# Optimization experiments

Measured on AMD Instinct MI355X. Metric: run time of the kernel, lower is better.

Reference implementation:

```python
import jax, jax.numpy as jnp
import numpy as np

NUM_HEADS = 8
EMBED_DIM = 512


def _attention(q, k, v, mask=None):
    # q,k,v: [batch, heads, Lq, d] / [batch, heads, Lk, d]
    s = jnp.einsum('bhqd,bhkd->bhqk', q, k)
    if mask is not None:
        s = jnp.where(mask, jnp.asarray(-1000.0, s.dtype), s)
    p = jax.nn.softmax(s, axis=-1)
    return jnp.einsum('bhqk,bhkd->bhqd', p, v)


def _t_mask(T, H):
    # True where attention is DISALLOWED (query frame t_q < key frame t_k)
    tq = jnp.arange(T)[:, None]
    tk = jnp.arange(T)[None, :]
    blocked = tq < tk  # [T, T]
    m = jnp.repeat(jnp.repeat(blocked, H, axis=0), H, axis=1)  # [T*H, T*H]
    return m


def setup_inputs() -> dict:
    key = jax.random.key(0)
    ks = jax.random.split(key, 10)
    B, T, H, W, E = 4, 4, 28, 28, EMBED_DIM
    N = T * H * W
    s_in = (2.0 / (E + 3 * E)) ** 0.5  # xavier-ish
    s_sq = (1.0 / E) ** 0.5
    return {
        'x': jax.random.normal(ks[0], (B, N, E), dtype=jnp.float32),
        'in_proj_weight': jax.random.normal(ks[1], (3 * E, E), dtype=jnp.float32) * s_in,
        'in_proj_bias': jnp.zeros((3 * E,), dtype=jnp.float32),
        'out_proj_w': jax.random.normal(ks[2], (E, E), dtype=jnp.float32) * s_sq,
        'out_proj_b': jnp.zeros((E,), dtype=jnp.float32),
        'in_proj_weight_t': jax.random.normal(ks[3], (E, E), dtype=jnp.float32) * s_sq,
        'in_proj_bias_t': jnp.zeros((E,), dtype=jnp.float32),
        'out_proj_t_w': jax.random.normal(ks[4], (E, E), dtype=jnp.float32) * s_sq,
        'out_proj_t_b': jnp.zeros((E,), dtype=jnp.float32),
        'alpha': 0.0001 * jnp.ones((E,), dtype=jnp.float32),
        'H': 28,
        'W': 28,
    }


def reference(x, in_proj_weight, in_proj_bias, out_proj_w, out_proj_b,
              in_proj_weight_t, in_proj_bias_t, out_proj_t_w, out_proj_t_b,
              alpha, H, W):
    B, N, C = x.shape
    nh = NUM_HEADS
    hc = C // nh
    T = N // (H * W)
    scale = hc ** (-0.5)

    # ---- spatial (per-frame) attention: _forward_2d ----
    qkv = x @ in_proj_weight.T + in_proj_bias            # [B, N, 3C]
    qkv = qkv.reshape(B, T, H * W, 3, nh, hc)
    qkv = qkv.transpose(3, 0, 1, 4, 2, 5).reshape(3, B * T, nh, H * W, hc)
    q, k, v = qkv[0], qkv[1], qkv[2]
    o = _attention(q * scale, k, v)                       # [B*T, nh, HW, hc]
    xs = o.transpose(0, 2, 1, 3).reshape(B, N, C)
    xs = xs @ out_proj_w.T + out_proj_b

    ks = jax.lax.stop_gradient(k)                         # detached cache
    vs = jax.lax.stop_gradient(v)

    # ---- axial temporal attention ----
    q_t = (x @ in_proj_weight_t.T + in_proj_bias_t) * scale  # [B, N, C]
    q_t = q_t.reshape(B, T, H, W, nh, hc)
    q_th = q_t.transpose(0, 3, 4, 1, 2, 5).reshape(B * W, nh, T * H, hc)
    q_tw = q_t.transpose(0, 2, 4, 1, 3, 5).reshape(B * H, nh, T * W, hc)

    k6 = ks.reshape(B, T, nh, H, W, hc)
    v6 = vs.reshape(B, T, nh, H, W, hc)
    k_th = k6.transpose(0, 4, 2, 1, 3, 5).reshape(B * W, nh, T * H, hc)
    k_tw = k6.transpose(0, 3, 2, 1, 4, 5).reshape(B * H, nh, T * W, hc)
    v_th = v6.transpose(0, 4, 2, 1, 3, 5).reshape(B * W, nh, T * H, hc)
    v_tw = v6.transpose(0, 3, 2, 1, 4, 5).reshape(B * H, nh, T * W, hc)

    o_th = _attention(q_th, k_th, v_th, _t_mask(T, H))    # [B*W, nh, T*H, hc]
    o_tw = _attention(q_tw, k_tw, v_tw, _t_mask(T, W))    # [B*H, nh, T*W, hc]

    o_th = o_th.reshape(B, W, nh, T, H, hc).transpose(0, 3, 4, 1, 2, 5).reshape(B, N, C)
    o_tw = o_tw.reshape(B, H, nh, T, W, hc).transpose(0, 3, 1, 4, 2, 5).reshape(B, N, C)

    x_t = (o_th + o_tw) @ out_proj_t_w.T + out_proj_t_b
    return xs + alpha * x_t
```

## Files before the change

kernel.cpp:

```cpp
#include <hip/hip_runtime.h>
#include <stdint.h>

#define NN   3136
#define MM   12544
#define SCALE 0.125f
#define KSCL  (0.125f * 1.44269504088896f)
#define MASKED (-30000.0f)

typedef __attribute__((ext_vector_type(8))) unsigned short ushort8;
typedef __attribute__((ext_vector_type(8))) short short8;
typedef __attribute__((ext_vector_type(4))) float floatx4;

__device__ __forceinline__ float b2f(unsigned short u) {
    union { unsigned int i; float f; } x; x.i = ((unsigned int)u) << 16; return x.f;
}
__device__ __forceinline__ unsigned short f2b(float f) {
    union { float f; unsigned int i; } x; x.f = f;
    unsigned int r = x.i + 0x7fffu + ((x.i >> 16) & 1u);
    return (unsigned short)(r >> 16);
}
__device__ __forceinline__ float fexp2(float x) {
    return __builtin_amdgcn_exp2f(x);
}
__device__ __forceinline__ void load8(const void* p, size_t e, int isf32, float o[8]) {
    if (isf32) {
        const float* f = (const float*)p + e;
        #pragma unroll
        for (int i = 0; i < 8; ++i) o[i] = f[i];
    } else {
        ushort8 u = *(const ushort8*)((const unsigned short*)p + e);
        #pragma unroll
        for (int i = 0; i < 8; ++i) o[i] = b2f(u[i]);
    }
}
__device__ __forceinline__ float load1(const void* p, int e, int isf32) {
    return isf32 ? ((const float*)p)[e] : b2f(((const unsigned short*)p)[e]);
}

__global__ void detect_dtype(const void* __restrict__ x, int* __restrict__ flagp)
{
    if (threadIdx.x == 0 && blockIdx.x == 0) {
        const unsigned short* u = (const unsigned short*)x;
        int c = 0;
        for (int i = 0; i < 512; ++i) {
            const float v = b2f(u[i]);
            if (!(v == v) || fabsf(v) > 1000.0f) ++c;
        }
        *flagp = (c >= 16) ? 1 : 0;
    }
}

__global__ __launch_bounds__(256) void convert_x(
    const int* __restrict__ flagp, const float* __restrict__ x,
    unsigned short* __restrict__ xb)
{
    if (!*flagp) return;
    const size_t i = ((size_t)blockIdx.x * 256 + threadIdx.x) * 8;
    const float4 a = *(const float4*)(x + i);
    const float4 b = *(const float4*)(x + i + 4);
    ushort8 o;
    o[0] = f2b(a.x); o[1] = f2b(a.y); o[2] = f2b(a.z); o[3] = f2b(a.w);
    o[4] = f2b(b.x); o[5] = f2b(b.y); o[6] = f2b(b.z); o[7] = f2b(b.w);
    *(ushort8*)(xb + i) = o;
}

__global__ __launch_bounds__(256) void convert_wp(
    const int* __restrict__ flagp, const void* __restrict__ Wi,
    const void* __restrict__ Wt, unsigned short* __restrict__ wp)
{
    const int isf32 = *flagp;
    const size_t e = ((size_t)blockIdx.x * 256 + threadIdx.x) * 8;
    const int row = (int)(e >> 9);
    const int col = (int)(e & 511);
    float v[8];
    if (row < 1536) load8(Wi, (size_t)row * 512 + col, isf32, v);
    else            load8(Wt, (size_t)(row - 1536) * 512 + col, isf32, v);
    if (row >= 512 && row < 1024) {
        #pragma unroll
        for (int u = 0; u < 8; ++u) v[u] *= KSCL;
    }
    ushort8 o;
    #pragma unroll
    for (int u = 0; u < 8; ++u) o[u] = f2b(v[u]);
    *(ushort8*)(wp + e) = o;
}

__global__ __launch_bounds__(256) void convert_wf(
    const int* __restrict__ flagp, const void* __restrict__ Wo,
    const void* __restrict__ Wto, const void* __restrict__ alp,
    unsigned short* __restrict__ qkv)
{
    const int isf32 = *flagp;
    const size_t e = ((size_t)blockIdx.x * 256 + threadIdx.x) * 8;
    const int row = (int)(e >> 10);
    const int k = (int)(e & 1023);
    float v[8];
    if (k < 512) load8(Wo, (size_t)row * 512 + k, isf32, v);
    else {
        const float a = load1(alp, row, isf32);
        load8(Wto, (size_t)row * 512 + (k - 512), isf32, v);
        #pragma unroll
        for (int u = 0; u < 8; ++u) v[u] *= a;
    }
    ushort8 o;
    #pragma unroll
    for (int u = 0; u < 8; ++u) o[u] = f2b(v[u]);
    *(ushort8*)(qkv + (size_t)row * 1536 + 512 + k) = o;
}

__global__ __launch_bounds__(256) void gemm_proj_mfma(
    const int* __restrict__ flagp, const void* __restrict__ x,
    const unsigned short* __restrict__ xb,
    const unsigned short* __restrict__ wp,
    const void* __restrict__ bi, const void* __restrict__ bt,
    unsigned short* __restrict__ qkv, unsigned short* __restrict__ qt)
{
    __shared__ unsigned short A_sh[128][40];
    __shared__ unsigned short B_sh[64][40];
    const int gid = blockIdx.x;
    const int mt = (gid >> 8) * 8 + (gid & 7);
    const int nt = (gid & 255) >> 3;
    if (mt >= 98) return;
    const int m0 = mt * 128, n0 = nt * 64;

    const int isf32 = *flagp;
    const unsigned short* A = isf32 ? xb : (const unsigned short*)x;
    const int tid = threadIdx.x, lane = tid & 63, wv = tid >> 6;
    const int lane15 = lane & 15, quad = lane >> 4;
    const int wm = wv >> 1, wn = wv & 1;

    const int ra = tid >> 1, ca = (tid & 1) * 16;
    const int rb = tid >> 2, cb = (tid & 3) * 8;
    const int nb = n0 + rb;

    floatx4 acc[4][2];
    #pragma unroll
    for (int i = 0; i < 4; ++i)
        #pragma unroll
        for (int j = 0; j < 2; ++j) acc[i][j] = (floatx4){0.f,0.f,0.f,0.f};

    for (int k0 = 0; k0 < 512; k0 += 32) {
        const unsigned short* ap = A + (size_t)(m0 + ra) * 512 + k0 + ca;
        *(ushort8*)&A_sh[ra][ca]     = *(const ushort8*)ap;
        *(ushort8*)&A_sh[ra][ca + 8] = *(const ushort8*)(ap + 8);
        *(ushort8*)&B_sh[rb][cb] = *(const ushort8*)(wp + (size_t)nb * 512 + k0 + cb);
        __syncthreads();

        short8 af[4], bf[2];
        #pragma unroll
        for (int i = 0; i < 4; ++i)
            af[i] = *(const short8*)&A_sh[wm * 64 + i * 16 + lane15][quad * 8];
        #pragma unroll
        for (int j = 0; j < 2; ++j)
            bf[j] = *(const short8*)&B_sh[wn * 32 + j * 16 + lane15][quad * 8];
        #pragma unroll
        for (int i = 0; i < 4; ++i)
            #pragma unroll
            for (int j = 0; j < 2; ++j)
                acc[i][j] = __builtin_amdgcn_mfma_f32_16x16x32_bf16(af[i], bf[j], acc[i][j], 0, 0, 0);
        __syncthreads();
    }

    #pragma unroll
    for (int j = 0; j < 2; ++j) {
        const int col = n0 + wn * 32 + j * 16 + lane15;
        float bias;
        unsigned short* dst;
        int stride;
        if (col < 1536) {
            bias = load1(bi, col, isf32);
            if (col >= 512 && col < 1024) bias *= KSCL;
            dst = qkv; stride = 1536;
        }
        else { bias = load1(bt, col - 1536, isf32); dst = qt; stride = 512; }
        const int cofs = (col < 1536) ? col : (col - 1536);
        #pragma unroll
        for (int i = 0; i < 4; ++i)
            #pragma unroll
            for (int r = 0; r < 4; ++r) {
                const int m = m0 + wm * 64 + i * 16 + quad * 4 + r;
                dst[(size_t)m * stride + cofs] = f2b(acc[i][j][r] + bias);
            }
    }
}

__global__ __launch_bounds__(256) void gemm_final_mfma(
    const int* __restrict__ flagp,
    const unsigned short* __restrict__ qkv, const unsigned short* __restrict__ qt,
    const void* __restrict__ bo, const void* __restrict__ bto,
    const void* __restrict__ alp, void* __restrict__ outp)
{
    __shared__ unsigned short A_sh[128][40];
    __shared__ unsigned short B_sh[64][40];
    const int gid = blockIdx.x;
    const int mt = (gid >> 6) * 8 + (gid & 7);
    const int nt = (gid & 63) >> 3;
    if (mt >= 98) return;
    const int m0 = mt * 128, n0 = nt * 64;

    const int isf32 = *flagp;
    const int tid = threadIdx.x, lane = tid & 63, wv = tid >> 6;
    const int lane15 = lane & 15, quad = lane >> 4;
    const int wm = wv >> 1, wn = wv & 1;

    const int ra = tid >> 1, ca = (tid & 1) * 16;
    const int rb = tid >> 2, cb = (tid & 3) * 8;
    const int nb = n0 + rb;

    floatx4 acc[4][2];
    #pragma unroll
    for (int i = 0; i < 4; ++i)
        #pragma unroll
        for (int j = 0; j < 2; ++j) acc[i][j] = (floatx4){0.f,0.f,0.f,0.f};

    for (int k0 = 0; k0 < 1024; k0 += 32) {
        const int m = m0 + ra;
        const unsigned short* ap = (k0 < 512)
            ? qkv + (size_t)m * 1536 + k0 + ca
            : qt  + (size_t)m * 512  + (k0 - 512) + ca;
        *(ushort8*)&A_sh[ra][ca]     = *(const ushort8*)ap;
        *(ushort8*)&A_sh[ra][ca + 8] = *(const ushort8*)(ap + 8);
        *(ushort8*)&B_sh[rb][cb] =
            *(const ushort8*)(qkv + (size_t)nb * 1536 + 512 + k0 + cb);
        __syncthreads();

        short8 af[4], bf[2];
        #pragma unroll
        for (int i = 0; i < 4; ++i)
            af[i] = *(const short8*)&A_sh[wm * 64 + i * 16 + lane15][quad * 8];
        #pragma unroll
        for (int j = 0; j < 2; ++j)
            bf[j] = *(const short8*)&B_sh[wn * 32 + j * 16 + lane15][quad * 8];
        #pragma unroll
        for (int i = 0; i < 4; ++i)
            #pragma unroll
            for (int j = 0; j < 2; ++j)
                acc[i][j] = __builtin_amdgcn_mfma_f32_16x16x32_bf16(af[i], bf[j], acc[i][j], 0, 0, 0);
        __syncthreads();
    }

    #pragma unroll
    for (int j = 0; j < 2; ++j) {
        const int col = n0 + wn * 32 + j * 16 + lane15;
        const float bias = load1(bo, col, isf32) + load1(alp, col, isf32) * load1(bto, col, isf32);
        #pragma unroll
        for (int i = 0; i < 4; ++i)
            #pragma unroll
            for (int r = 0; r < 4; ++r) {
                const int m = m0 + wm * 64 + i * 16 + quad * 4 + r;
                const float val = acc[i][j][r] + bias;
                const size_t idx = (size_t)m * 512 + col;
                if (isf32) ((float*)outp)[idx] = val;
                else       ((unsigned short*)outp)[idx] = f2b(val);
            }
    }
}

__global__ __launch_bounds__(512) void attn_spatial_mfma(unsigned short* __restrict__ qkv)
{
    __shared__ unsigned short K_sh[64][72];
    __shared__ unsigned short VT_sh[64][72];
    __shared__ unsigned short P_sh[8][16][72];

    const int tid = threadIdx.x, lane = tid & 63, wv = tid >> 6;
    const int lane15 = lane & 15, quad = lane >> 4;

    const int gid = blockIdx.x;
    const int xcd = gid & 7, kk = gid >> 3;
    const int grp = xcd * 16 + kk / 7;
    const int qb  = kk % 7;
    const int head = grp & 7, bt = grp >> 3;

    const int t0 = qb * 8 + wv;
    const bool act = (t0 < 49);
    const int q0 = act ? t0 * 16 : 0;
    const int frame0 = bt * 784;

    short8 q_lo = {0,0,0,0,0,0,0,0}, q_hi = {0,0,0,0,0,0,0,0};
    if (act) {
        const unsigned short* qp = qkv + (size_t)(frame0 + q0 + lane15) * 1536 + head * 64 + quad * 8;
        q_lo = *(const short8*)qp;
        q_hi = *(const short8*)(qp + 32);
    }

    floatx4 accO[4] = {{0.f,0.f,0.f,0.f},{0.f,0.f,0.f,0.f},{0.f,0.f,0.f,0.f},{0.f,0.f,0.f,0.f}};
    float ls[4] = {0.f, 0.f, 0.f, 0.f};

    const int key_l = tid & 63;
    const int cs    = (tid >> 6) * 8;
    const int swzp  = (lane15 >> 2) << 4;

    for (int kt = 0; kt < 13; ++kt) {
        __syncthreads();
        const int key = kt * 64 + key_l;
        ushort8 k8 = {0,0,0,0,0,0,0,0}, v8 = {0,0,0,0,0,0,0,0};
        if (key < 784) {
            const unsigned short* kp = qkv + (size_t)(frame0 + key) * 1536 + head * 64 + cs;
            k8 = *(const ushort8*)(kp + 512);
            v8 = *(const ushort8*)(kp + 1024);
        }
        *(ushort8*)&K_sh[key_l][cs] = k8;
        #pragma unroll
        for (int u = 0; u < 8; ++u) VT_sh[cs + u][key_l] = v8[u];
        __syncthreads();

        floatx4 s[4];
        #pragma unroll
        for (int st = 0; st < 4; ++st) {
            const short8 kfl = *(const short8*)&K_sh[st * 16 + lane15][quad * 8];
            const short8 kfh = *(const short8*)&K_sh[st * 16 + lane15][32 + quad * 8];
            floatx4 a = {0.f,0.f,0.f,0.f};
            a = __builtin_amdgcn_mfma_f32_16x16x32_bf16(q_lo, kfl, a, 0, 0, 0);
            a = __builtin_amdgcn_mfma_f32_16x16x32_bf16(q_hi, kfh, a, 0, 0, 0);
            s[st] = a;
        }

        const bool tail = (kt == 12);
        #pragma unroll
        for (int st = 0; st < 4; ++st)
            #pragma unroll
            for (int r = 0; r < 4; ++r) {
                const float v = (tail && st >= 1) ? MASKED : s[st][r];
                const float p = fexp2(v);
                ls[r] += p;
                P_sh[wv][quad * 4 + r][(st * 16 + lane15) ^ (quad << 4)] = f2b(p);
            }

        #pragma unroll
        for (int kc = 0; kc < 2; ++kc) {
            const short8 pf = *(const short8*)&P_sh[wv][lane15][(kc * 32 + quad * 8) ^ swzp];
            #pragma unroll
            for (int nt = 0; nt < 4; ++nt) {
                const short8 vf = *(const short8*)&VT_sh[nt * 16 + lane15][kc * 32 + quad * 8];
                accO[nt] = __builtin_amdgcn_mfma_f32_16x16x32_bf16(pf, vf, accO[nt], 0, 0, 0);
            }
        }
    }

    #pragma unroll
    for (int off = 1; off < 16; off <<= 1)
        #pragma unroll
        for (int r = 0; r < 4; ++r)
            ls[r] += __shfl_xor(ls[r], off, 64);

    if (act) {
        #pragma unroll
        for (int nt = 0; nt < 4; ++nt)
            #pragma unroll
            for (int r = 0; r < 4; ++r) {
                const int qrow = q0 + quad * 4 + r;
                qkv[(size_t)(frame0 + qrow) * 1536 + head * 64 + nt * 16 + lane15]
                    = f2b(accO[nt][r] / ls[r]);
            }
    }
}

__global__ __launch_bounds__(448) void attn_axial(
    const unsigned short* __restrict__ qkv, const unsigned short* __restrict__ qtu,
    const unsigned short* __restrict__ oth, unsigned short* __restrict__ outp,
    const int pass)
{
    __shared__ unsigned short K_sh[112][72];
    __shared__ unsigned short VT_sh[64][136];
    __shared__ unsigned short P_sh[7][16][136];

    const int tid = threadIdx.x, lane = tid & 63, wv = tid >> 6;
    const int lane15 = lane & 15, quad = lane >> 4;
    const int b = blockIdx.x / 28, pos = blockIdx.x % 28;
    const int head = blockIdx.y;
    const int swzp = (lane15 >> 2) << 4;

    for (int idx = tid; idx < 1024; idx += 448) {
        const int j = idx >> 3, cc = (idx & 7) << 3;
        if (j < 112) {
            const int tk = j / 28, rk = j % 28;
            const int n_k = tk * 784 + (pass == 0 ? rk * 28 + pos : pos * 28 + rk);
            const unsigned short* kp = qkv + (size_t)(b * NN + n_k) * 1536 + 512 + head * 64 + cc;
            const ushort8 k8 = *(const ushort8*)kp;
            const ushort8 v8 = *(const ushort8*)(kp + 512);
            *(ushort8*)&K_sh[j][cc] = k8;
            #pragma unroll
            for (int u = 0; u < 8; ++u) VT_sh[cc + u][j ^ cc] = v8[u];
        } else {
            #pragma unroll
            for (int u = 0; u < 8; ++u) VT_sh[cc + u][j ^ cc] = 0;
        }
    }
    __syncthreads();

    const int tile = wv;
    {
        const int iq = tile * 16 + lane15;
        const int tq_q = iq / 28, rq = iq % 28;
        const int n_q = tq_q * 784 + (pass == 0 ? rq * 28 + pos : pos * 28 + rq);
        const size_t qaddr = (size_t)(b * NN + n_q) * 512 + head * 64;
        const short8 q_lo = *(const short8*)(qtu + qaddr + quad * 8);
        const short8 q_hi = *(const short8*)(qtu + qaddr + 32 + quad * 8);

        floatx4 s[7];
        #pragma unroll
        for (int st = 0; st < 7; ++st) {
            const short8 kfl = *(const short8*)&K_sh[st * 16 + lane15][quad * 8];
            const short8 kfh = *(const short8*)&K_sh[st * 16 + lane15][32 + quad * 8];
            floatx4 acc = {0.f,0.f,0.f,0.f};
            acc = __builtin_amdgcn_mfma_f32_16x16x32_bf16(q_lo, kfl, acc, 0, 0, 0);
            acc = __builtin_amdgcn_mfma_f32_16x16x32_bf16(q_hi, kfh, acc, 0, 0, 0);
            s[st] = acc;
        }

        int tq_row[4];
        #pragma unroll
        for (int r = 0; r < 4; ++r) tq_row[r] = (tile * 16 + quad * 4 + r) / 28;
        float l[4] = {0.f, 0.f, 0.f, 0.f};
        #pragma unroll
        for (int st = 0; st < 7; ++st) {
            const int tk = (st * 16 + lane15) / 28;
            #pragma unroll
            for (int r = 0; r < 4; ++r) {
                const float v = (tk <= tq_row[r]) ? s[st][r] : MASKED;
                const float p = fexp2(v);
                s[st][r] = p;
                l[r] += p;
            }
        }
        #pragma unroll
        for (int off = 1; off < 16; off <<= 1)
            #pragma unroll
            for (int r = 0; r < 4; ++r)
                l[r] += __shfl_xor(l[r], off, 64);

        #pragma unroll
        for (int r = 0; r < 4; ++r) {
            const int row = quad * 4 + r;
            #pragma unroll
            for (int st = 0; st < 7; ++st)
                P_sh[wv][row][(st * 16 + lane15) ^ (quad << 4)] = f2b(s[st][r]);
            P_sh[wv][row][(112 + lane15) ^ (quad << 4)] = 0;
        }

        floatx4 accO[4] = {{0.f,0.f,0.f,0.f},{0.f,0.f,0.f,0.f},{0.f,0.f,0.f,0.f},{0.f,0.f,0.f,0.f}};
        #pragma unroll
        for (int kc = 0; kc < 4; ++kc) {
            const short8 pf = *(const short8*)&P_sh[wv][lane15][(kc * 32 + quad * 8) ^ swzp];
            #pragma unroll
            for (int nt = 0; nt < 4; ++nt) {
                const int row = nt * 16 + lane15;
                const short8 vf = *(const short8*)&VT_sh[row][(kc * 32 + quad * 8) ^ ((row >> 3) << 3)];
                accO[nt] = __builtin_amdgcn_mfma_f32_16x16x32_bf16(pf, vf, accO[nt], 0, 0, 0);
            }
        }

        #pragma unroll
        for (int r = 0; r < 4; ++r) {
            const int io = tile * 16 + quad * 4 + r;
            const int to = io / 28, ro = io % 28;
            const int n_o = to * 784 + (pass == 0 ? ro * 28 + pos : pos * 28 + ro);
            const size_t oaddr = (size_t)(b * NN + n_o) * 512 + head * 64;
            #pragma unroll
            for (int nt = 0; nt < 4; ++nt) {
                float o = accO[nt][r] / l[r];
                if (pass == 1) o += b2f(oth[oaddr + nt * 16 + lane15]);
                outp[oaddr + nt * 16 + lane15] = f2b(o);
            }
        }
    }
}

__global__ void fill_val(unsigned short* o, unsigned short v, int n) {
    const int i = blockIdx.x * 256 + threadIdx.x;
    if (i < n) o[i] = v;
}

extern "C" void kernel_launch(void* const* d_in, const int* in_sizes, int n_in,
                              void* d_out, int out_size, void* d_ws, size_t ws_size,
                              hipStream_t stream)
{
    const void* x   = d_in[0];
    const void* Wi  = d_in[1];
    const void* bi  = d_in[2];
    const void* Wo  = d_in[3];
    const void* bo  = d_in[4];
    const void* Wt  = d_in[5];
    const void* bt  = d_in[6];
    const void* Wto = d_in[7];
    const void* bto = d_in[8];
    const void* alp = d_in[9];

    const size_t QKV_ELEMS = (size_t)MM * 1536;
    const size_t QT_ELEMS  = (size_t)MM * 512;
    const size_t FLAG_OFF  = (QKV_ELEMS + QT_ELEMS) * 2;
    const size_t NEED      = FLAG_OFF + 256;

    if (ws_size < NEED) {
        fill_val<<<dim3((out_size + 255) / 256), dim3(256), 0, stream>>>(
            (unsigned short*)d_out, (unsigned short)0x3f80, out_size);
        return;
    }

    unsigned short* qkv = (unsigned short*)d_ws;
    unsigned short* qt  = qkv + QKV_ELEMS;
    int* flagp = (int*)((char*)d_ws + FLAG_OFF);
    unsigned short* oth = (unsigned short*)d_out;
    unsigned short* xb  = oth + (size_t)MM * 512;
    unsigned short* wp  = oth;

    dim3 blk(256);
    detect_dtype<<<dim3(1), dim3(64), 0, stream>>>(x, flagp);
    convert_x<<<dim3(MM * 512 / (256 * 8)), blk, 0, stream>>>(flagp, (const float*)x, xb);
    convert_wp<<<dim3(2048 * 512 / (256 * 8)), blk, 0, stream>>>(flagp, Wi, Wt, wp);
    gemm_proj_mfma<<<dim3(13 * 256), blk, 0, stream>>>(
        flagp, x, xb, wp, bi, bt, qkv, qt);
    attn_spatial_mfma<<<dim3(112 * 8), dim3(512), 0, stream>>>(qkv);
    attn_axial<<<dim3(112, 8), dim3(448), 0, stream>>>(qkv, qt, nullptr, oth, 0);
    attn_axial<<<dim3(112, 8), dim3(448), 0, stream>>>(qkv, qt, oth, qt, 1);
    convert_wf<<<dim3(512 * 1024 / (256 * 8)), blk, 0, stream>>>(flagp, Wo, Wto, alp, qkv);
    gemm_final_mfma<<<dim3(13 * 64), blk, 0, stream>>>(
        flagp, qkv, qt, bo, bto, alp, d_out);
}
```

Before: 297.4 us.

## Stage spatial-attention K/V in two large LDS halves with XOR swizzling

The spatial attention kernel now loads 448 keys and then the remaining 336 keys (padded to 384) of K and transposed V into large shared-memory buffers. This replaces thirteen 64-key tiles that each needed two barriers, so the kernel hits far fewer __syncthreads. K and VT stores and reads are XOR-swizzled to avoid LDS bank conflicts without padding. The cost is much larger LDS use per block (roughly 64KB+ for K_sh plus VT_sh), which limits occupancy to one block per CU. Load and compute are also no longer overlapped across tiles.

Result: slower. 308.9 us (+3.9%).

```diff
diff --git a/kernel.cpp b/kernel.cpp
--- a/kernel.cpp
+++ b/kernel.cpp
@@ -258,8 +258,8 @@
 
 __global__ __launch_bounds__(512) void attn_spatial_mfma(unsigned short* __restrict__ qkv)
 {
-    __shared__ unsigned short K_sh[64][72];
-    __shared__ unsigned short VT_sh[64][72];
+    __shared__ unsigned short K_sh[448][72];
+    __shared__ unsigned short VT_sh[64][448];
     __shared__ unsigned short P_sh[8][16][72];
 
     const int tid = threadIdx.x, lane = tid & 63, wv = tid >> 6;
@@ -286,55 +286,73 @@
     floatx4 accO[4] = {{0.f,0.f,0.f,0.f},{0.f,0.f,0.f,0.f},{0.f,0.f,0.f,0.f},{0.f,0.f,0.f,0.f}};
     float ls[4] = {0.f, 0.f, 0.f, 0.f};
 
-    const int key_l = tid & 63;
-    const int cs    = (tid >> 6) * 8;
-    const int swzp  = (lane15 >> 2) << 4;
-
-    for (int kt = 0; kt < 13; ++kt) {
-        __syncthreads();
-        const int key = kt * 64 + key_l;
-        ushort8 k8 = {0,0,0,0,0,0,0,0}, v8 = {0,0,0,0,0,0,0,0};
-        if (key < 784) {
-            const unsigned short* kp = qkv + (size_t)(frame0 + key) * 1536 + head * 64 + cs;
-            k8 = *(const ushort8*)(kp + 512);
-            v8 = *(const ushort8*)(kp + 1024);
-        }
-        *(ushort8*)&K_sh[key_l][cs] = k8;
-        #pragma unroll
-        for (int u = 0; u < 8; ++u) VT_sh[cs + u][key_l] = v8[u];
-        __syncthreads();
-
+    const int swzp = (lane15 >> 2) << 4;
+    const int r7l  = lane15 & 7;
+
+    auto chunk = [&](int c, bool msk) {
         floatx4 s[4];
         #pragma unroll
         for (int st = 0; st < 4; ++st) {
-            const short8 kfl = *(const short8*)&K_sh[st * 16 + lane15][quad * 8];
-            const short8 kfh = *(const short8*)&K_sh[st * 16 + lane15][32 + quad * 8];
+            const int row = c * 64 + st * 16 + lane15;
+            const short8 kfl = *(const short8*)&K_sh[row][(quad ^ r7l) * 8];
+            const short8 kfh = *(const short8*)&K_sh[row][((quad + 4) ^ r7l) * 8];
             floatx4 a = {0.f,0.f,0.f,0.f};
             a = __builtin_amdgcn_mfma_f32_16x16x32_bf16(q_lo, kfl, a, 0, 0, 0);
             a = __builtin_amdgcn_mfma_f32_16x16x32_bf16(q_hi, kfh, a, 0, 0, 0);
             s[st] = a;
         }
-
-        const bool tail = (kt == 12);
         #pragma unroll
         for (int st = 0; st < 4; ++st)
             #pragma unroll
             for (int r = 0; r < 4; ++r) {
-                const float v = (tail && st >= 1) ? MASKED : s[st][r];
+                const float v = (msk && st >= 1) ? MASKED : s[st][r];
                 const float p = fexp2(v);
                 ls[r] += p;
                 P_sh[wv][quad * 4 + r][(st * 16 + lane15) ^ (quad << 4)] = f2b(p);
             }
-
         #pragma unroll
         for (int kc = 0; kc < 2; ++kc) {
             const short8 pf = *(const short8*)&P_sh[wv][lane15][(kc * 32 + quad * 8) ^ swzp];
             #pragma unroll
             for (int nt = 0; nt < 4; ++nt) {
-                const short8 vf = *(const short8*)&VT_sh[nt * 16 + lane15][kc * 32 + quad * 8];
+                const int vrow = nt * 16 + lane15;
+                const short8 vf = *(const short8*)
+                    &VT_sh[vrow][(c * 64 + kc * 32 + quad * 8) ^ ((vrow >> 3) << 3)];
                 accO[nt] = __builtin_amdgcn_mfma_f32_16x16x32_bf16(pf, vf, accO[nt], 0, 0, 0);
             }
         }
+    };
+
+    for (int idx = tid; idx < 448 * 8; idx += 512) {
+        const int j = idx >> 3, cc = idx & 7, d0 = cc * 8;
+        const unsigned short* kp = qkv + (size_t)(frame0 + j) * 1536 + head * 64 + d0;
+        const ushort8 k8 = *(const ushort8*)(kp + 512);
+        const ushort8 v8 = *(const ushort8*)(kp + 1024);
+        *(ushort8*)&K_sh[j][(cc ^ (j & 7)) * 8] = k8;
+        #pragma unroll
+        for (int u = 0; u < 8; ++u) VT_sh[d0 + u][j ^ (cc << 3)] = v8[u];
+    }
+    __syncthreads();
+    if (act) {
+        for (int c = 0; c < 7; ++c) chunk(c, false);
+    }
+    __syncthreads();
+
+    for (int idx = tid; idx < 384 * 8; idx += 512) {
+        const int j = idx >> 3, cc = idx & 7, d0 = cc * 8;
+        ushort8 k8 = {0,0,0,0,0,0,0,0}, v8 = {0,0,0,0,0,0,0,0};
+        if (j < 336) {
+            const unsigned short* kp = qkv + (size_t)(frame0 + 448 + j) * 1536 + head * 64 + d0;
+            k8 = *(const ushort8*)(kp + 512);
+            v8 = *(const ushort8*)(kp + 1024);
+        }
+        *(ushort8*)&K_sh[j][(cc ^ (j & 7)) * 8] = k8;
+        #pragma unroll
+        for (int u = 0; u < 8; ++u) VT_sh[d0 + u][j ^ (cc << 3)] = v8[u];
+    }
+    __syncthreads();
+    if (act) {
+        for (int c = 0; c < 6; ++c) chunk(c, c == 5);
     }
 
     #pragma unroll
```

## Fuse spatial attention with first axial pass and merge pre-conversion kernels

Applied to the files above, without the earlier changes.

Spatial attention and the first axial attention pass become one launch. Interleaved slabs of blocks run either the spatial or the axial body out of a shared 64000-byte static LDS buffer. The two are independent: spatial writes only the Q slots, and axial reads only K/V and qt. The x conversion and the weight conversion kernels are also merged into one launch. The intent is to cut launch overhead and tail idle time and to let the two attention workloads overlap. The cost is a larger fixed LDS footprint per block, which may lower the occupancy of the spatial blocks.

Measured after the change: 319.2 us. 7.3% more time.

```diff
diff --git a/kernel.cpp b/kernel.cpp
--- a/kernel.cpp
+++ b/kernel.cpp
@@ -50,39 +50,39 @@
     }
 }
 
-__global__ __launch_bounds__(256) void convert_x(
+__global__ __launch_bounds__(256) void pre_convert(
     const int* __restrict__ flagp, const float* __restrict__ x,
-    unsigned short* __restrict__ xb)
-{
-    if (!*flagp) return;
-    const size_t i = ((size_t)blockIdx.x * 256 + threadIdx.x) * 8;
-    const float4 a = *(const float4*)(x + i);
-    const float4 b = *(const float4*)(x + i + 4);
-    ushort8 o;
-    o[0] = f2b(a.x); o[1] = f2b(a.y); o[2] = f2b(a.z); o[3] = f2b(a.w);
-    o[4] = f2b(b.x); o[5] = f2b(b.y); o[6] = f2b(b.z); o[7] = f2b(b.w);
-    *(ushort8*)(xb + i) = o;
-}
-
-__global__ __launch_bounds__(256) void convert_wp(
-    const int* __restrict__ flagp, const void* __restrict__ Wi,
-    const void* __restrict__ Wt, unsigned short* __restrict__ wp)
-{
+    unsigned short* __restrict__ xb,
+    const void* __restrict__ Wi, const void* __restrict__ Wt,
+    unsigned short* __restrict__ wp)
+{
+    const int g = blockIdx.x;
     const int isf32 = *flagp;
-    const size_t e = ((size_t)blockIdx.x * 256 + threadIdx.x) * 8;
-    const int row = (int)(e >> 9);
-    const int col = (int)(e & 511);
-    float v[8];
-    if (row < 1536) load8(Wi, (size_t)row * 512 + col, isf32, v);
-    else            load8(Wt, (size_t)(row - 1536) * 512 + col, isf32, v);
-    if (row >= 512 && row < 1024) {
-        #pragma unroll
-        for (int u = 0; u < 8; ++u) v[u] *= KSCL;
-    }
-    ushort8 o;
-    #pragma unroll
-    for (int u = 0; u < 8; ++u) o[u] = f2b(v[u]);
-    *(ushort8*)(wp + e) = o;
+    if (g < 3136) {
+        if (!isf32) return;
+        const size_t i = ((size_t)g * 256 + threadIdx.x) * 8;
+        const float4 a = *(const float4*)(x + i);
+        const float4 b = *(const float4*)(x + i + 4);
+        ushort8 o;
+        o[0] = f2b(a.x); o[1] = f2b(a.y); o[2] = f2b(a.z); o[3] = f2b(a.w);
+        o[4] = f2b(b.x); o[5] = f2b(b.y); o[6] = f2b(b.z); o[7] = f2b(b.w);
+        *(ushort8*)(xb + i) = o;
+    } else {
+        const size_t e = ((size_t)(g - 3136) * 256 + threadIdx.x) * 8;
+        const int row = (int)(e >> 9);
+        const int col = (int)(e & 511);
+        float v[8];
+        if (row < 1536) load8(Wi, (size_t)row * 512 + col, isf32, v);
+        else            load8(Wt, (size_t)(row - 1536) * 512 + col, isf32, v);
+        if (row >= 512 && row < 1024) {
+            #pragma unroll
+            for (int u = 0; u < 8; ++u) v[u] *= KSCL;
+        }
+        ushort8 o;
+        #pragma unroll
+        for (int u = 0; u < 8; ++u) o[u] = f2b(v[u]);
+        *(ushort8*)(wp + e) = o;
+    }
 }
 
 __global__ __launch_bounds__(256) void convert_wf(
@@ -256,17 +256,17 @@
     }
 }
 
-__global__ __launch_bounds__(512) void attn_spatial_mfma(unsigned short* __restrict__ qkv)
-{
-    __shared__ unsigned short K_sh[64][72];
-    __shared__ unsigned short VT_sh[64][72];
-    __shared__ unsigned short P_sh[8][16][72];
+__device__ __forceinline__ void spatial_body(
+    unsigned short* __restrict__ qkv, const int sub, unsigned char* smem)
+{
+    unsigned short (*K_sh)[72]      = (unsigned short (*)[72])smem;
+    unsigned short (*VT_sh)[72]     = (unsigned short (*)[72])(smem + 9216);
+    unsigned short (*P_sh)[16][72]  = (unsigned short (*)[16][72])(smem + 18432);
 
     const int tid = threadIdx.x, lane = tid & 63, wv = tid >> 6;
     const int lane15 = lane & 15, quad = lane >> 4;
 
-    const int gid = blockIdx.x;
-    const int xcd = gid & 7, kk = gid >> 3;
+    const int xcd = sub & 7, kk = sub >> 3;
     const int grp = xcd * 16 + kk / 7;
     const int qb  = kk % 7;
     const int head = grp & 7, bt = grp >> 3;
@@ -355,26 +355,25 @@
     }
 }
 
-__global__ __launch_bounds__(448) void attn_axial(
+__device__ __forceinline__ void axial0_body(
     const unsigned short* __restrict__ qkv, const unsigned short* __restrict__ qtu,
-    const unsigned short* __restrict__ oth, unsigned short* __restrict__ outp,
-    const int pass)
-{
-    __shared__ unsigned short K_sh[112][72];
-    __shared__ unsigned short VT_sh[64][136];
-    __shared__ unsigned short P_sh[7][16][136];
+    unsigned short* __restrict__ outp, const int sub, unsigned char* smem)
+{
+    unsigned short (*K_sh)[72]       = (unsigned short (*)[72])smem;
+    unsigned short (*VT_sh)[136]     = (unsigned short (*)[136])(smem + 16128);
+    unsigned short (*P_sh)[16][136]  = (unsigned short (*)[16][136])(smem + 33536);
 
     const int tid = threadIdx.x, lane = tid & 63, wv = tid >> 6;
     const int lane15 = lane & 15, quad = lane >> 4;
-    const int b = blockIdx.x / 28, pos = blockIdx.x % 28;
-    const int head = blockIdx.y;
+    const int head = sub / 112, xy = sub % 112;
+    const int b = xy / 28, pos = xy % 28;
     const int swzp = (lane15 >> 2) << 4;
 
-    for (int idx = tid; idx < 1024; idx += 448) {
+    for (int idx = tid; idx < 1024; idx += 512) {
         const int j = idx >> 3, cc = (idx & 7) << 3;
         if (j < 112) {
             const int tk = j / 28, rk = j % 28;
-            const int n_k = tk * 784 + (pass == 0 ? rk * 28 + pos : pos * 28 + rk);
+            const int n_k = tk * 784 + rk * 28 + pos;
             const unsigned short* kp = qkv + (size_t)(b * NN + n_k) * 1536 + 512 + head * 64 + cc;
             const ushort8 k8 = *(const ushort8*)kp;
             const ushort8 v8 = *(const ushort8*)(kp + 512);
@@ -388,11 +387,12 @@
     }
     __syncthreads();
 
+    if (wv >= 7) return;
     const int tile = wv;
     {
         const int iq = tile * 16 + lane15;
         const int tq_q = iq / 28, rq = iq % 28;
-        const int n_q = tq_q * 784 + (pass == 0 ? rq * 28 + pos : pos * 28 + rq);
+        const int n_q = tq_q * 784 + rq * 28 + pos;
         const size_t qaddr = (size_t)(b * NN + n_q) * 512 + head * 64;
         const short8 q_lo = *(const short8*)(qtu + qaddr + quad * 8);
         const short8 q_hi = *(const short8*)(qtu + qaddr + 32 + quad * 8);
@@ -454,12 +454,131 @@
         for (int r = 0; r < 4; ++r) {
             const int io = tile * 16 + quad * 4 + r;
             const int to = io / 28, ro = io % 28;
-            const int n_o = to * 784 + (pass == 0 ? ro * 28 + pos : pos * 28 + ro);
+            const int n_o = to * 784 + ro * 28 + pos;
+            const size_t oaddr = (size_t)(b * NN + n_o) * 512 + head * 64;
+            #pragma unroll
+            for (int nt = 0; nt < 4; ++nt)
+                outp[oaddr + nt * 16 + lane15] = f2b(accO[nt][r] / l[r]);
+        }
+    }
+}
+
+__global__ __launch_bounds__(512) void attn_fused(
+    unsigned short* __restrict__ qkv, const unsigned short* __restrict__ qtu,
+    unsigned short* __restrict__ oth)
+{
+    __shared__ __align__(16) unsigned char smem[64000];
+    const int g = blockIdx.x;
+    const int slab = g >> 3, lane8 = g & 7;
+    const int sub = (slab >> 1) * 8 + lane8;
+    if ((slab & 1) == 0) spatial_body(qkv, sub, smem);
+    else                 axial0_body(qkv, qtu, oth, sub, smem);
+}
+
+__global__ __launch_bounds__(448) void attn_axial1(
+    const unsigned short* __restrict__ qkv, const unsigned short* __restrict__ qtu,
+    const unsigned short* __restrict__ oth, unsigned short* __restrict__ outp)
+{
+    __shared__ unsigned short K_sh[112][72];
+    __shared__ unsigned short VT_sh[64][136];
+    __shared__ unsigned short P_sh[7][16][136];
+
+    const int tid = threadIdx.x, lane = tid & 63, wv = tid >> 6;
+    const int lane15 = lane & 15, quad = lane >> 4;
+    const int b = blockIdx.x / 28, pos = blockIdx.x % 28;
+    const int head = blockIdx.y;
+    const int swzp = (lane15 >> 2) << 4;
+
+    for (int idx = tid; idx < 1024; idx += 448) {
+        const int j = idx >> 3, cc = (idx & 7) << 3;
+        if (j < 112) {
+            const int tk = j / 28, rk = j % 28;
+            const int n_k = tk * 784 + pos * 28 + rk;
+            const unsigned short* kp = qkv + (size_t)(b * NN + n_k) * 1536 + 512 + head * 64 + cc;
+            const ushort8 k8 = *(const ushort8*)kp;
+            const ushort8 v8 = *(const ushort8*)(kp + 512);
+            *(ushort8*)&K_sh[j][cc] = k8;
+            #pragma unroll
+            for (int u = 0; u < 8; ++u) VT_sh[cc + u][j ^ cc] = v8[u];
+        } else {
+            #pragma unroll
+            for (int u = 0; u < 8; ++u) VT_sh[cc + u][j ^ cc] = 0;
+        }
+    }
+    __syncthreads();
+
+    const int tile = wv;
+    {
+        const int iq = tile * 16 + lane15;
+        const int tq_q = iq / 28, rq = iq % 28;
+        const int n_q = tq_q * 784 + pos * 28 + rq;
+        const size_t qaddr = (size_t)(b * NN + n_q) * 512 + head * 64;
+        const short8 q_lo = *(const short8*)(qtu + qaddr + quad * 8);
+        const short8 q_hi = *(const short8*)(qtu + qaddr + 32 + quad * 8);
+
+        floatx4 s[7];
+        #pragma unroll
+        for (int st = 0; st < 7; ++st) {
+            const short8 kfl = *(const short8*)&K_sh[st * 16 + lane15][quad * 8];
+            const short8 kfh = *(const short8*)&K_sh[st * 16 + lane15][32 + quad * 8];
+            floatx4 acc = {0.f,0.f,0.f,0.f};
+            acc = __builtin_amdgcn_mfma_f32_16x16x32_bf16(q_lo, kfl, acc, 0, 0, 0);
+            acc = __builtin_amdgcn_mfma_f32_16x16x32_bf16(q_hi, kfh, acc, 0, 0, 0);
+            s[st] = acc;
+        }
+
+        int tq_row[4];
+        #pragma unroll
+        for (int r = 0; r < 4; ++r) tq_row[r] = (tile * 16 + quad * 4 + r) / 28;
+        float l[4] = {0.f, 0.f, 0.f, 0.f};
+        #pragma unroll
+        for (int st = 0; st < 7; ++st) {
+            const int tk = (st * 16 + lane15) / 28;
+            #pragma unroll
+            for (int r = 0; r < 4; ++r) {
+                const float v = (tk <= tq_row[r]) ? s[st][r] : MASKED;
+                const float p = fexp2(v);
+                s[st][r] = p;
+                l[r] += p;
+            }
+        }
+        #pragma unroll
+        for (int off = 1; off < 16; off <<= 1)
+            #pragma unroll
+            for (int r = 0; r < 4; ++r)
+                l[r] += __shfl_xor(l[r], off, 64);
+
+        #pragma unroll
+        for (int r = 0; r < 4; ++r) {
+            const int row = quad * 4 + r;
+            #pragma unroll
+            for (int st = 0; st < 7; ++st)
+                P_sh[wv][row][(st * 16 + lane15) ^ (quad << 4)] = f2b(s[st][r]);
+            P_sh[wv][row][(112 + lane15) ^ (quad << 4)] = 0;
+        }
+
+        floatx4 accO[4] = {{0.f,0.f,0.f,0.f},{0.f,0.f,0.f,0.f},{0.f,0.f,0.f,0.f},{0.f,0.f,0.f,0.f}};
+        #pragma unroll
+        for (int kc = 0; kc < 4; ++kc) {
+            const short8 pf = *(const short8*)&P_sh[wv][lane15][(kc * 32 + quad * 8) ^ swzp];
+            #pragma unroll
+            for (int nt = 0; nt < 4; ++nt) {
+                const int row = nt * 16 + lane15;
+                const short8 vf = *(const short8*)&VT_sh[row][(kc * 32 + quad * 8) ^ ((row >> 3) << 3)];
+                accO[nt] = __builtin_amdgcn_mfma_f32_16x16x32_bf16(pf, vf, accO[nt], 0, 0, 0);
+            }
+        }
+
+        #pragma unroll
+        for (int r = 0; r < 4; ++r) {
+            const int io = tile * 16 + quad * 4 + r;
+            const int to = io / 28, ro = io % 28;
+            const int n_o = to * 784 + pos * 28 + ro;
             const size_t oaddr = (size_t)(b * NN + n_o) * 512 + head * 64;
             #pragma unroll
             for (int nt = 0; nt < 4; ++nt) {
                 float o = accO[nt][r] / l[r];
-                if (pass == 1) o += b2f(oth[oaddr + nt * 16 + lane15]);
+                o += b2f(oth[oaddr + nt * 16 + lane15]);
                 outp[oaddr + nt * 16 + lane15] = f2b(o);
             }
         }
@@ -506,13 +625,12 @@
 
     dim3 blk(256);
     detect_dtype<<<dim3(1), dim3(64), 0, stream>>>(x, flagp);
-    convert_x<<<dim3(MM * 512 / (256 * 8)), blk, 0, stream>>>(flagp, (const float*)x, xb);
-    convert_wp<<<dim3(2048 * 512 / (256 * 8)), blk, 0, stream>>>(flagp, Wi, Wt, wp);
+    pre_convert<<<dim3(3136 + 512), blk, 0, stream>>>(
+        flagp, (const float*)x, xb, Wi, Wt, wp);
     gemm_proj_mfma<<<dim3(13 * 256), blk, 0, stream>>>(
         flagp, x, xb, wp, bi, bt, qkv, qt);
-    attn_spatial_mfma<<<dim3(112 * 8), dim3(512), 0, stream>>>(qkv);
-    attn_axial<<<dim3(112, 8), dim3(448), 0, stream>>>(qkv, qt, nullptr, oth, 0);
-    attn_axial<<<dim3(112, 8), dim3(448), 0, stream>>>(qkv, qt, oth, qt, 1);
+    attn_fused<<<dim3(1792), dim3(512), 0, stream>>>(qkv, qt, oth);
+    attn_axial1<<<dim3(112, 8), dim3(448), 0, stream>>>(qkv, qt, oth, qt);
     convert_wf<<<dim3(512 * 1024 / (256 * 8)), blk, 0, stream>>>(flagp, Wo, Wto, alp, qkv);
     gemm_final_mfma<<<dim3(13 * 64), blk, 0, stream>>>(
         flagp, qkv, qt, bo, bto, alp, d_out);
```

## Double-buffer K/V tiles in spatial attention and merge conversion kernels

Applied to the files above, without the earlier changes.

The spatial attention kernel now keeps two shared-memory buffers for K and V^T. It prefetches the next key tile into registers while computing on the current one, which removes one barrier per iteration and hides global-load latency behind the MFMA work. Separately, the x and weight conversion kernels are merged into a single launch to save one kernel launch. The cost is doubled LDS for the K/V buffers, which could reduce occupancy, plus higher register pressure from the prefetched values.

Result: faster. 283.9 us (-4.6%).

```diff
diff --git a/kernel.cpp b/kernel.cpp
--- a/kernel.cpp
+++ b/kernel.cpp
@@ -50,39 +50,39 @@
     }
 }
 
-__global__ __launch_bounds__(256) void convert_x(
+__global__ __launch_bounds__(256) void pre_convert(
     const int* __restrict__ flagp, const float* __restrict__ x,
-    unsigned short* __restrict__ xb)
-{
-    if (!*flagp) return;
-    const size_t i = ((size_t)blockIdx.x * 256 + threadIdx.x) * 8;
-    const float4 a = *(const float4*)(x + i);
-    const float4 b = *(const float4*)(x + i + 4);
-    ushort8 o;
-    o[0] = f2b(a.x); o[1] = f2b(a.y); o[2] = f2b(a.z); o[3] = f2b(a.w);
-    o[4] = f2b(b.x); o[5] = f2b(b.y); o[6] = f2b(b.z); o[7] = f2b(b.w);
-    *(ushort8*)(xb + i) = o;
-}
-
-__global__ __launch_bounds__(256) void convert_wp(
-    const int* __restrict__ flagp, const void* __restrict__ Wi,
-    const void* __restrict__ Wt, unsigned short* __restrict__ wp)
-{
+    unsigned short* __restrict__ xb,
+    const void* __restrict__ Wi, const void* __restrict__ Wt,
+    unsigned short* __restrict__ wp)
+{
+    const int g = blockIdx.x;
     const int isf32 = *flagp;
-    const size_t e = ((size_t)blockIdx.x * 256 + threadIdx.x) * 8;
-    const int row = (int)(e >> 9);
-    const int col = (int)(e & 511);
-    float v[8];
-    if (row < 1536) load8(Wi, (size_t)row * 512 + col, isf32, v);
-    else            load8(Wt, (size_t)(row - 1536) * 512 + col, isf32, v);
-    if (row >= 512 && row < 1024) {
-        #pragma unroll
-        for (int u = 0; u < 8; ++u) v[u] *= KSCL;
-    }
-    ushort8 o;
-    #pragma unroll
-    for (int u = 0; u < 8; ++u) o[u] = f2b(v[u]);
-    *(ushort8*)(wp + e) = o;
+    if (g < 3136) {
+        if (!isf32) return;
+        const size_t i = ((size_t)g * 256 + threadIdx.x) * 8;
+        const float4 a = *(const float4*)(x + i);
+        const float4 b = *(const float4*)(x + i + 4);
+        ushort8 o;
+        o[0] = f2b(a.x); o[1] = f2b(a.y); o[2] = f2b(a.z); o[3] = f2b(a.w);
+        o[4] = f2b(b.x); o[5] = f2b(b.y); o[6] = f2b(b.z); o[7] = f2b(b.w);
+        *(ushort8*)(xb + i) = o;
+    } else {
+        const size_t e = ((size_t)(g - 3136) * 256 + threadIdx.x) * 8;
+        const int row = (int)(e >> 9);
+        const int col = (int)(e & 511);
+        float v[8];
+        if (row < 1536) load8(Wi, (size_t)row * 512 + col, isf32, v);
+        else            load8(Wt, (size_t)(row - 1536) * 512 + col, isf32, v);
+        if (row >= 512 && row < 1024) {
+            #pragma unroll
+            for (int u = 0; u < 8; ++u) v[u] *= KSCL;
+        }
+        ushort8 o;
+        #pragma unroll
+        for (int u = 0; u < 8; ++u) o[u] = f2b(v[u]);
+        *(ushort8*)(wp + e) = o;
+    }
 }
 
 __global__ __launch_bounds__(256) void convert_wf(
@@ -258,8 +258,8 @@
 
 __global__ __launch_bounds__(512) void attn_spatial_mfma(unsigned short* __restrict__ qkv)
 {
-    __shared__ unsigned short K_sh[64][72];
-    __shared__ unsigned short VT_sh[64][72];
+    __shared__ unsigned short K_sh[2][64][72];
+    __shared__ unsigned short VT_sh[2][64][72];
     __shared__ unsigned short P_sh[8][16][72];
 
     const int tid = threadIdx.x, lane = tid & 63, wv = tid >> 6;
@@ -290,25 +290,34 @@
     const int cs    = (tid >> 6) * 8;
     const int swzp  = (lane15 >> 2) << 4;
 
+    {
+        const unsigned short* kp = qkv + (size_t)(frame0 + key_l) * 1536 + head * 64 + cs;
+        const ushort8 k8 = *(const ushort8*)(kp + 512);
+        const ushort8 v8 = *(const ushort8*)(kp + 1024);
+        *(ushort8*)&K_sh[0][key_l][cs] = k8;
+        #pragma unroll
+        for (int u = 0; u < 8; ++u) VT_sh[0][cs + u][key_l] = v8[u];
+    }
+    __syncthreads();
+
     for (int kt = 0; kt < 13; ++kt) {
-        __syncthreads();
-        const int key = kt * 64 + key_l;
-        ushort8 k8 = {0,0,0,0,0,0,0,0}, v8 = {0,0,0,0,0,0,0,0};
-        if (key < 784) {
-            const unsigned short* kp = qkv + (size_t)(frame0 + key) * 1536 + head * 64 + cs;
-            k8 = *(const ushort8*)(kp + 512);
-            v8 = *(const ushort8*)(kp + 1024);
-        }
-        *(ushort8*)&K_sh[key_l][cs] = k8;
-        #pragma unroll
-        for (int u = 0; u < 8; ++u) VT_sh[cs + u][key_l] = v8[u];
-        __syncthreads();
+        const int cur = kt & 1;
+
+        ushort8 nk8 = {0,0,0,0,0,0,0,0}, nv8 = {0,0,0,0,0,0,0,0};
+        if (kt < 12) {
+            const int nkey = (kt + 1) * 64 + key_l;
+            if (nkey < 784) {
+                const unsigned short* kp = qkv + (size_t)(frame0 + nkey) * 1536 + head * 64 + cs;
+                nk8 = *(const ushort8*)(kp + 512);
+                nv8 = *(const ushort8*)(kp + 1024);
+            }
+        }
 
         floatx4 s[4];
         #pragma unroll
         for (int st = 0; st < 4; ++st) {
-            const short8 kfl = *(const short8*)&K_sh[st * 16 + lane15][quad * 8];
-            const short8 kfh = *(const short8*)&K_sh[st * 16 + lane15][32 + quad * 8];
+            const short8 kfl = *(const short8*)&K_sh[cur][st * 16 + lane15][quad * 8];
+            const short8 kfh = *(const short8*)&K_sh[cur][st * 16 + lane15][32 + quad * 8];
             floatx4 a = {0.f,0.f,0.f,0.f};
             a = __builtin_amdgcn_mfma_f32_16x16x32_bf16(q_lo, kfl, a, 0, 0, 0);
             a = __builtin_amdgcn_mfma_f32_16x16x32_bf16(q_hi, kfh, a, 0, 0, 0);
@@ -331,10 +340,17 @@
             const short8 pf = *(const short8*)&P_sh[wv][lane15][(kc * 32 + quad * 8) ^ swzp];
             #pragma unroll
             for (int nt = 0; nt < 4; ++nt) {
-                const short8 vf = *(const short8*)&VT_sh[nt * 16 + lane15][kc * 32 + quad * 8];
+                const short8 vf = *(const short8*)&VT_sh[cur][nt * 16 + lane15][kc * 32 + quad * 8];
                 accO[nt] = __builtin_amdgcn_mfma_f32_16x16x32_bf16(pf, vf, accO[nt], 0, 0, 0);
             }
         }
+
+        if (kt < 12) {
+            *(ushort8*)&K_sh[cur ^ 1][key_l][cs] = nk8;
+            #pragma unroll
+            for (int u = 0; u < 8; ++u) VT_sh[cur ^ 1][cs + u][key_l] = nv8[u];
+        }
+        __syncthreads();
     }
 
     #pragma unroll
@@ -506,8 +522,8 @@
 
     dim3 blk(256);
     detect_dtype<<<dim3(1), dim3(64), 0, stream>>>(x, flagp);
-    convert_x<<<dim3(MM * 512 / (256 * 8)), blk, 0, stream>>>(flagp, (const float*)x, xb);
-    convert_wp<<<dim3(2048 * 512 / (256 * 8)), blk, 0, stream>>>(flagp, Wi, Wt, wp);
+    pre_convert<<<dim3(3136 + 512), blk, 0, stream>>>(
+        flagp, (const float*)x, xb, Wi, Wt, wp);
     gemm_proj_mfma<<<dim3(13 * 256), blk, 0, stream>>>(
         flagp, x, xb, wp, bi, bt, qkv, qt);
     attn_spatial_mfma<<<dim3(112 * 8), dim3(512), 0, stream>>>(qkv);
```
